# Optimization experiments

Measured on AMD Instinct MI355X. Metric: run time of the kernel, lower is better.

Reference implementation:

```python
import jax, jax.numpy as jnp
import numpy as np

EMBED_DIM = 1024
NUM_HEADS = 16
GQA = 4
KV_HEADS = NUM_HEADS // GQA          # 4
HEAD_DIM = EMBED_DIM // NUM_HEADS    # 64
KV_EMBED = KV_HEADS * HEAD_DIM       # 512
EPS = 1e-3
B, T = 2, 1024


def monotonic_attention(probs):
    """Many-to-many monotonic attention over sigmoid probs.

    probs: (..., Tq, Tk) in (0,1).
    Recurrence: phi[0] = onehot(key 0);
      phi[i, j] = p[i-1, j] * phi[i-1, j] + (1 - p[i, j-1]) * phi[i, j-1].
    The inner (j) recurrence is a first-order linear recurrence solved with
    an associative scan; the outer (i) recurrence uses lax.scan.
    """
    p = jnp.clip(probs, EPS, 1.0 - EPS)
    p_t = jnp.moveaxis(p, -2, 0)  # (Tq, ..., Tk)
    init = jnp.zeros(p_t.shape[1:], p.dtype).at[..., 0].set(1.0)

    def combine(x, y):
        A1, b1 = x
        A2, b2 = y
        return (A1 * A2, b1 * A2 + b2)

    def step(phi_prev, rows):
        p_prev, p_cur = rows
        a = phi_prev * p_prev                    # mass arriving from row above
        q = 1.0 - p_cur                          # stay-in-row (move right) prob
        A = jnp.concatenate([jnp.zeros_like(q[..., :1]), q[..., :-1]], axis=-1)
        _, phi = jax.lax.associative_scan(combine, (A, a), axis=-1)
        return phi, phi

    _, phis = jax.lax.scan(step, init, (p_t[:-1], p_t[1:]))
    phis = jnp.concatenate([init[None], phis], axis=0)  # (Tq, ..., Tk)
    return jnp.moveaxis(phis, 0, -2)


def setup_inputs() -> dict:
    key = jax.random.key(0)
    ks = jax.random.split(key, 5)
    scale_in = (2.0 / (EMBED_DIM + 2 * KV_EMBED + EMBED_DIM)) ** 0.5  # xavier-ish
    scale_out = (2.0 / (2 * EMBED_DIM)) ** 0.5
    return {
        "query": jax.random.normal(ks[0], (B, T, EMBED_DIM), jnp.float32),
        "key": jax.random.normal(ks[1], (B, T, EMBED_DIM), jnp.float32),
        "value": jax.random.normal(ks[2], (B, T, EMBED_DIM), jnp.float32),
        "in_proj_weight": jax.random.normal(ks[3], (EMBED_DIM + 2 * KV_EMBED, EMBED_DIM), jnp.float32) * scale_in,
        "in_proj_bias": jnp.zeros((EMBED_DIM + 2 * KV_EMBED,), jnp.float32),
        "out_proj_weight": jax.random.normal(ks[4], (EMBED_DIM, EMBED_DIM), jnp.float32) * scale_out,
        "out_proj_bias": jnp.zeros((EMBED_DIM,), jnp.float32),
    }


def reference(query, key, value, in_proj_weight, in_proj_bias, out_proj_weight, out_proj_bias):
    qw = in_proj_weight[:EMBED_DIM]
    kw = in_proj_weight[EMBED_DIM:EMBED_DIM + KV_EMBED]
    vw = in_proj_weight[EMBED_DIM + KV_EMBED:]
    qb = in_proj_bias[:EMBED_DIM]
    kb = in_proj_bias[EMBED_DIM:EMBED_DIM + KV_EMBED]
    vb = in_proj_bias[EMBED_DIM + KV_EMBED:]

    b, tq, _ = query.shape
    tk = key.shape[1]
    xq = query @ qw.T + qb   # (B, Tq, E)
    xk = key @ kw.T + kb     # (B, Tk, KV_EMBED)
    xv = value @ vw.T + vb   # (B, Tk, KV_EMBED)

    # (B, G, H, Tq, C) and (B, H, Tk, C)
    xq = xq.reshape(b, tq, GQA, KV_HEADS, HEAD_DIM).transpose(0, 2, 3, 1, 4)
    xk = xk.reshape(b, tk, KV_HEADS, HEAD_DIM).transpose(0, 2, 1, 3)
    xv = xv.reshape(b, tk, KV_HEADS, HEAD_DIM).transpose(0, 2, 1, 3)

    attn = jnp.einsum("bghqc,bhkc->bghqk", xq, xk)
    attn = monotonic_attention(jax.nn.sigmoid(attn))
    xo = jnp.einsum("bghqk,bhkc->bghqc", attn, xv)
    xo = xo.transpose(0, 3, 1, 2, 4).reshape(b, tq, EMBED_DIM)
    return xo @ out_proj_weight.T + out_proj_bias
```

## Files before the change

### kernel.cpp

```cpp
#include <hip/hip_runtime.h>
#include <cstddef>
#include <cstdint>

#define TSEQ 1024

typedef __attribute__((ext_vector_type(8))) short short8;
typedef __attribute__((ext_vector_type(4))) float floatx4;

static constexpr size_t OFF_XQ  = 0;
static constexpr size_t OFF_XK  = (size_t)2 * 1024 * 1024;
static constexpr size_t OFF_XVT = OFF_XK + (size_t)512 * 1024;
static constexpr size_t OFF_XO  = OFF_XVT + (size_t)512 * 1024;
static constexpr size_t OFF_P   = OFF_XO + (size_t)2 * 1024 * 1024;


__device__ __forceinline__ void cvt_hi_lo(float x, unsigned short& hi,
                                          unsigned short& lo) {
  unsigned u = __float_as_uint(x);
  unsigned rh = (u + 0x7FFFu + ((u >> 16) & 1u)) & 0xFFFF0000u;
  hi = (unsigned short)(rh >> 16);
  float xl = x - __uint_as_float(rh);
  unsigned ul = __float_as_uint(xl);
  unsigned rl = ul + 0x7FFFu + ((ul >> 16) & 1u);
  lo = (unsigned short)(rl >> 16);
}

__device__ __forceinline__ int diagrow(int r, int cblk) {
  return ((((r >> 2) + cblk) & 255) << 2) | (r & 3);
}

typedef unsigned short lds_tile_t[40];

template <int EPI, int ADIAG, int CDIAG>
__device__ __forceinline__ void mfma_nt_core(
    const float* __restrict__ A, int lda,
    const float* __restrict__ B, int ldb,
    float* __restrict__ C, int ldc, int K,
    const float* __restrict__ bias,
    int bm, int bn,
    lds_tile_t* __restrict__ Ah, lds_tile_t* __restrict__ Al,
    lds_tile_t* __restrict__ Bh, lds_tile_t* __restrict__ Bl)
{
  const int tid  = threadIdx.x;
  const int lane = tid & 63;
  const int wave = tid >> 6;
  const int m16  = lane & 15;
  const int quad = lane >> 4;

  const int srow = tid >> 2;
  const int skq  = (tid & 3) << 3;

  floatx4 acc[4];
#pragma unroll
  for (int c = 0; c < 4; ++c) acc[c] = (floatx4){0.f, 0.f, 0.f, 0.f};

  for (int k0 = 0; k0 < K; k0 += 32) {
    {
      const int kq = k0 + skq;
      int arow = bm + srow;
      if (ADIAG) arow = diagrow(arow, kq >> 4);
      const float* ap = A + (size_t)arow * lda + kq;
      const float* bp = B + (size_t)(bn + srow) * ldb + kq;
      float av[8] __attribute__((aligned(16)));
      float bv[8] __attribute__((aligned(16)));
      *(float4*)&av[0] = *(const float4*)(ap);
      *(float4*)&av[4] = *(const float4*)(ap + 4);
      *(float4*)&bv[0] = *(const float4*)(bp);
      *(float4*)&bv[4] = *(const float4*)(bp + 4);
      short8 vah, valo, vbh, vblo;
#pragma unroll
      for (int e = 0; e < 8; ++e) {
        unsigned short h, l;
        cvt_hi_lo(av[e], h, l);
        vah[e] = (short)h; valo[e] = (short)l;
        cvt_hi_lo(bv[e], h, l);
        vbh[e] = (short)h; vblo[e] = (short)l;
      }
      *(short8*)&Ah[srow][skq] = vah;
      *(short8*)&Al[srow][skq] = valo;
      *(short8*)&Bh[srow][skq] = vbh;
      *(short8*)&Bl[srow][skq] = vblo;
    }
    __syncthreads();

    const int arow = (wave << 4) + m16;
    const short8 a_h = *(const short8*)&Ah[arow][quad << 3];
    const short8 a_l = *(const short8*)&Al[arow][quad << 3];
#pragma unroll
    for (int c = 0; c < 4; ++c) {
      const int brow = (c << 4) + m16;
      const short8 b_h = *(const short8*)&Bh[brow][quad << 3];
      const short8 b_l = *(const short8*)&Bl[brow][quad << 3];
      acc[c] = __builtin_amdgcn_mfma_f32_16x16x32_bf16(a_h, b_h, acc[c], 0, 0, 0);
      acc[c] = __builtin_amdgcn_mfma_f32_16x16x32_bf16(a_h, b_l, acc[c], 0, 0, 0);
      acc[c] = __builtin_amdgcn_mfma_f32_16x16x32_bf16(a_l, b_h, acc[c], 0, 0, 0);
    }
    __syncthreads();
  }

#pragma unroll
  for (int c = 0; c < 4; ++c) {
#pragma unroll
    for (int r = 0; r < 4; ++r) {
      const int row = (wave << 4) + (quad << 2) + r;
      const int col = (c << 4) + m16;
      float v = acc[c][r];
      if (EPI == 0) { if (bias) v += bias[bn + col]; }
      if (EPI == 1) { v += bias[bm + row]; }
      if (EPI == 2) {
        v = 1.0f / (1.0f + __expf(v));
        v = fminf(fmaxf(v, 0.001f), 0.999f);
      }
      int crow = bm + row;
      if (CDIAG) crow = diagrow(crow, (bn + col) >> 4);
      C[(size_t)crow * ldc + (bn + col)] = v;
    }
  }
}

#define DECL_GEMM_SMEM                                          \
  __shared__ __align__(16) unsigned short Ah[64][40];           \
  __shared__ __align__(16) unsigned short Al[64][40];           \
  __shared__ __align__(16) unsigned short Bh[64][40];           \
  __shared__ __align__(16) unsigned short Bl[64][40];

__global__ __launch_bounds__(256) void inproj_k(
    const float* __restrict__ query, const float* __restrict__ key,
    const float* __restrict__ value, const float* __restrict__ ipw,
    const float* __restrict__ ipb,
    float* __restrict__ XQ, float* __restrict__ XK, float* __restrict__ XVt)
{
  DECL_GEMM_SMEM
  const int id = blockIdx.x;
  if (id < 512) {
    mfma_nt_core<0, 0, 0>(query, 1024, ipw, 1024, XQ, 1024, 1024, ipb,
                          (id >> 4) << 6, (id & 15) << 6, Ah, Al, Bh, Bl);
  } else if (id < 640) {
    const int j = id - 512;
    mfma_nt_core<0, 0, 0>(key, 1024, ipw + ((size_t)1 << 20), 1024,
                          XK, 256, 1024, ipb + 1024,
                          (j >> 2) << 6, (j & 3) << 6, Ah, Al, Bh, Bl);
  } else {
    const int j = id - 640;
    const int b = j >> 6;
    mfma_nt_core<1, 0, 0>(ipw + (size_t)1280 * 1024, 1024,
                          value + ((size_t)b << 20), 1024,
                          XVt + (size_t)b * 256 * 1024, 1024, 1024,
                          ipb + 1280,
                          ((j >> 4) & 3) << 6, (j & 15) << 6, Ah, Al, Bh, Bl);
  }
}

__global__ __launch_bounds__(256) void gemm_nt_mfma_k(
    const float* __restrict__ A, int lda, const float* __restrict__ W, int ldw,
    const float* __restrict__ bias, float* __restrict__ C, int ldc, int K)
{
  DECL_GEMM_SMEM
  mfma_nt_core<0, 0, 0>(A, lda, W, ldw, C, ldc, K, bias,
                        blockIdx.y << 6, blockIdx.x << 6, Ah, Al, Bh, Bl);
}

__global__ __launch_bounds__(256) void scores_mfma_k(
    const float* __restrict__ XQ, const float* __restrict__ XK,
    float* __restrict__ P)
{
  DECL_GEMM_SMEM
  const int z = blockIdx.z;
  const int b = z >> 4;
  mfma_nt_core<2, 0, 1>(XQ + ((size_t)b << 20) + ((size_t)(z & 15) << 6), 1024,
                        XK + (size_t)b * TSEQ * 256 + ((size_t)(z & 3) << 6), 256,
                        P + ((size_t)z << 20), 1024, 64, nullptr,
                        blockIdx.y << 6, blockIdx.x << 6, Ah, Al, Bh, Bl);
}

__global__ __launch_bounds__(256) void pv_mfma_k(
    const float* __restrict__ P, const float* __restrict__ XVt,
    float* __restrict__ XO)
{
  DECL_GEMM_SMEM
  const int z = blockIdx.z;
  const int b = z >> 4;
  mfma_nt_core<0, 1, 0>(P + ((size_t)z << 20), 1024,
                        XVt + (size_t)b * 256 * 1024 + (size_t)(z & 3) * 64 * 1024, 1024,
                        XO + ((size_t)b << 20) + ((size_t)(z & 15) << 6), 1024,
                        1024, nullptr,
                        blockIdx.y << 6, blockIdx.x << 6, Ah, Al, Bh, Bl);
}

__global__ __launch_bounds__(64) void mono_rec_k(float* __restrict__ P)
{
  const int z = blockIdx.x;
  float* __restrict__ Pz = P + ((size_t)z << 20);
  const int t = threadIdx.x;
  const int col0 = t << 4;

  float b[16];
#pragma unroll
  for (int c = 0; c < 16; ++c) b[c] = 0.0f;
  float phi15h[4], q15h[4];
#pragma unroll
  for (int k = 0; k < 4; ++k) { phi15h[k] = 0.0f; q15h[k] = 0.0f; }

  float pA[4][16], pB[4][16];

#pragma unroll
  for (int k = 0; k < 4; ++k) {
    const float* lp = Pz + (k << 10) + col0;
#pragma unroll
    for (int q = 0; q < 4; ++q)
      *(float4*)&pA[k][4 * q] = *(const float4*)(lp + 4 * q);
  }

  auto step = [&](int s, float (&pcur)[4][16], float (&pnext)[4][16]) {
    float phiL[4], qL[4];
#pragma unroll
    for (int k = 0; k < 4; ++k) {
      phiL[k] = __shfl_up(phi15h[k], 1);
      qL[k]   = __shfl_up(q15h[k], 1);
    }

    {
      const float* np = Pz + ((size_t)((s + 1) & 255) << 12) + col0;
#pragma unroll
      for (int k = 0; k < 4; ++k)
#pragma unroll
        for (int q = 0; q < 4; ++q)
          *(float4*)&pnext[k][4 * q] = *(const float4*)(np + (k << 10) + 4 * q);
    }

    const int g = s - t;
    if (g >= 0 && g < 256) {
      float* sp = Pz + ((size_t)(s & 255) << 12) + col0;
      float phi[16];
#pragma unroll
      for (int k = 0; k < 4; ++k) {
        const float* qk = pcur[k];
        if (g == 0 && k == 0) {
#pragma unroll
          for (int c = 0; c < 16; ++c) phi[c] = 0.0f;
          if (t == 0) phi[0] = 1.0f;
        } else {
          const float H0 = (t == 0) ? 0.0f : qL[k];
          float x = fmaf(H0, phiL[k], b[0]);
          phi[0] = x;
#pragma unroll
          for (int c = 1; c < 16; ++c) {
            x = fmaf(qk[c - 1], x, b[c]);
            phi[c] = x;
          }
        }
#pragma unroll
        for (int c = 0; c < 16; ++c) b[c] = fmaf(-qk[c], phi[c], phi[c]);
        q15h[k]   = qk[15];
        phi15h[k] = phi[15];
#pragma unroll
        for (int q = 0; q < 4; ++q)
          *(float4*)(sp + (k << 10) + 4 * q) = *(float4*)&phi[4 * q];
      }
    }
  };

  for (int s0 = 0; s0 < 320; s0 += 2) {
    step(s0, pA, pB);
    step(s0 + 1, pB, pA);
  }
}

extern "C" void kernel_launch(void* const* d_in, const int* in_sizes, int n_in,
                              void* d_out, int out_size, void* d_ws, size_t ws_size,
                              hipStream_t stream)
{
  const float* query = (const float*)d_in[0];
  const float* key   = (const float*)d_in[1];
  const float* value = (const float*)d_in[2];
  const float* ipw   = (const float*)d_in[3];
  const float* ipb   = (const float*)d_in[4];
  const float* opw   = (const float*)d_in[5];
  const float* opb   = (const float*)d_in[6];
  float* out = (float*)d_out;
  float* ws  = (float*)d_ws;

  float* XQ  = ws + OFF_XQ;
  float* XK  = ws + OFF_XK;
  float* XVt = ws + OFF_XVT;
  float* XO  = ws + OFF_XO;
  float* P   = ws + OFF_P;

  inproj_k<<<dim3(768), 256, 0, stream>>>(
      query, key, value, ipw, ipb, XQ, XK, XVt);

  scores_mfma_k<<<dim3(16, 16, 32), 256, 0, stream>>>(XQ, XK, P);

  mono_rec_k<<<dim3(32), dim3(64), 0, stream>>>(P);

  pv_mfma_k<<<dim3(1, 16, 32), 256, 0, stream>>>(P, XVt, XO);

  gemm_nt_mfma_k<<<dim3(16, 32), 256, 0, stream>>>(
      XO, 1024, opw, 1024, opb, out, 1024, 1024);
}
```

Measured before the change: 483.9 us.

## Widen monotonic recurrence to 256 threads with LDS wave-boundary handoff

The monotonic-attention wavefront kernel now runs 256 threads per head, with each thread owning 4 columns instead of 16. Carries between waves pass through double-buffered shared memory guarded by a block barrier on every step. The diagonal storage layout of P changes from 16-column to 4-column granularity, and the scores and PV GEMM loaders are adjusted to match. The goal is more parallelism and a shorter serial chain per step, at the cost of more wavefront steps (512 instead of 320) and a barrier in each one.

Result: slower. 495.2 us (+2.3%).

```diff
diff --git a/kernel.cpp b/kernel.cpp
--- a/kernel.cpp
+++ b/kernel.cpp
@@ -25,8 +25,8 @@
   lo = (unsigned short)(rl >> 16);
 }
 
-__device__ __forceinline__ int diagrow(int r, int cblk) {
-  return ((((r >> 2) + cblk) & 255) << 2) | (r & 3);
+__device__ __forceinline__ int diagrow4(int r, int c) {
+  return ((((r >> 2) + (c >> 2)) & 255) << 2) | (r & 3);
 }
 
 typedef unsigned short lds_tile_t[40];
@@ -57,14 +57,23 @@
   for (int k0 = 0; k0 < K; k0 += 32) {
     {
       const int kq = k0 + skq;
-      int arow = bm + srow;
-      if (ADIAG) arow = diagrow(arow, kq >> 4);
-      const float* ap = A + (size_t)arow * lda + kq;
+      const float* ap;
+      const float* ap2;
+      if (ADIAG) {
+        const int r  = bm + srow;
+        const int a0 = diagrow4(r, kq);
+        const int a1 = diagrow4(r, kq + 4);
+        ap  = A + (size_t)a0 * lda + kq;
+        ap2 = A + (size_t)a1 * lda + (kq + 4);
+      } else {
+        ap  = A + (size_t)(bm + srow) * lda + kq;
+        ap2 = ap + 4;
+      }
       const float* bp = B + (size_t)(bn + srow) * ldb + kq;
       float av[8] __attribute__((aligned(16)));
       float bv[8] __attribute__((aligned(16)));
       *(float4*)&av[0] = *(const float4*)(ap);
-      *(float4*)&av[4] = *(const float4*)(ap + 4);
+      *(float4*)&av[4] = *(const float4*)(ap2);
       *(float4*)&bv[0] = *(const float4*)(bp);
       *(float4*)&bv[4] = *(const float4*)(bp + 4);
       short8 vah, valo, vbh, vblo;
@@ -112,7 +121,7 @@
         v = fminf(fmaxf(v, 0.001f), 0.999f);
       }
       int crow = bm + row;
-      if (CDIAG) crow = diagrow(crow, (bn + col) >> 4);
+      if (CDIAG) crow = diagrow4(bm + row, bn + col);
       C[(size_t)crow * ldc + (bn + col)] = v;
     }
   }
@@ -187,80 +196,103 @@
                         blockIdx.y << 6, blockIdx.x << 6, Ah, Al, Bh, Bl);
 }
 
-__global__ __launch_bounds__(64) void mono_rec_k(float* __restrict__ P)
+#define MONO_BAR() do {                                          \
+    asm volatile("s_waitcnt lgkmcnt(0)" ::: "memory");           \
+    __builtin_amdgcn_sched_barrier(0);                           \
+    asm volatile("s_barrier" ::: "memory");                      \
+    __builtin_amdgcn_sched_barrier(0);                           \
+  } while (0)
+
+__global__ __launch_bounds__(256, 1) void mono_rec_k(float* __restrict__ P)
 {
   const int z = blockIdx.x;
   float* __restrict__ Pz = P + ((size_t)z << 20);
-  const int t = threadIdx.x;
-  const int col0 = t << 4;
-
-  float b[16];
-#pragma unroll
-  for (int c = 0; c < 16; ++c) b[c] = 0.0f;
-  float phi15h[4], q15h[4];
-#pragma unroll
-  for (int k = 0; k < 4; ++k) { phi15h[k] = 0.0f; q15h[k] = 0.0f; }
-
-  float pA[4][16], pB[4][16];
-
-#pragma unroll
-  for (int k = 0; k < 4; ++k) {
-    const float* lp = Pz + (k << 10) + col0;
-#pragma unroll
-    for (int q = 0; q < 4; ++q)
-      *(float4*)&pA[k][4 * q] = *(const float4*)(lp + 4 * q);
-  }
-
-  auto step = [&](int s, float (&pcur)[4][16], float (&pnext)[4][16]) {
+  const int tid = threadIdx.x;
+  const int u = tid;
+  const int w = tid >> 6;
+  const int l = tid & 63;
+
+  __shared__ float BndP[2][3][4];
+  __shared__ float BndQ[2][3][4];
+
+  float b[4];
+#pragma unroll
+  for (int c = 0; c < 4; ++c) b[c] = 0.0f;
+  float phi3h[4], q3h[4];
+#pragma unroll
+  for (int k = 0; k < 4; ++k) { phi3h[k] = 0.0f; q3h[k] = 0.0f; }
+
+  float pA[4][4], pB[4][4];
+
+#pragma unroll
+  for (int k = 0; k < 4; ++k)
+    *(float4*)&pA[k][0] = *(const float4*)(Pz + (k << 10) + (u << 2));
+
+  auto step = [&](int s, float (&pcur)[4][4], float (&pnext)[4][4]) {
     float phiL[4], qL[4];
 #pragma unroll
     for (int k = 0; k < 4; ++k) {
-      phiL[k] = __shfl_up(phi15h[k], 1);
-      qL[k]   = __shfl_up(q15h[k], 1);
+      phiL[k] = __shfl_up(phi3h[k], 1);
+      qL[k]   = __shfl_up(q3h[k], 1);
+    }
+    if (l == 0 && w > 0) {
+#pragma unroll
+      for (int k = 0; k < 4; ++k) {
+        phiL[k] = BndP[(s + 1) & 1][w - 1][k];
+        qL[k]   = BndQ[(s + 1) & 1][w - 1][k];
+      }
     }
 
     {
-      const float* np = Pz + ((size_t)((s + 1) & 255) << 12) + col0;
+      const float* np = Pz + ((size_t)((s + 1) & 255) << 12) + (u << 2);
 #pragma unroll
       for (int k = 0; k < 4; ++k)
-#pragma unroll
-        for (int q = 0; q < 4; ++q)
-          *(float4*)&pnext[k][4 * q] = *(const float4*)(np + (k << 10) + 4 * q);
-    }
-
-    const int g = s - t;
+        *(float4*)&pnext[k][0] = *(const float4*)(np + (k << 10));
+    }
+
+    const int g = s - u;
     if (g >= 0 && g < 256) {
-      float* sp = Pz + ((size_t)(s & 255) << 12) + col0;
-      float phi[16];
+      float phim[4][4];
 #pragma unroll
       for (int k = 0; k < 4; ++k) {
         const float* qk = pcur[k];
+        float* phi = phim[k];
         if (g == 0 && k == 0) {
 #pragma unroll
-          for (int c = 0; c < 16; ++c) phi[c] = 0.0f;
-          if (t == 0) phi[0] = 1.0f;
+          for (int c = 0; c < 4; ++c) phi[c] = 0.0f;
+          if (u == 0) phi[0] = 1.0f;
         } else {
-          const float H0 = (t == 0) ? 0.0f : qL[k];
+          const float H0 = (u == 0) ? 0.0f : qL[k];
           float x = fmaf(H0, phiL[k], b[0]);
           phi[0] = x;
 #pragma unroll
-          for (int c = 1; c < 16; ++c) {
+          for (int c = 1; c < 4; ++c) {
             x = fmaf(qk[c - 1], x, b[c]);
             phi[c] = x;
           }
         }
 #pragma unroll
-        for (int c = 0; c < 16; ++c) b[c] = fmaf(-qk[c], phi[c], phi[c]);
-        q15h[k]   = qk[15];
-        phi15h[k] = phi[15];
-#pragma unroll
-        for (int q = 0; q < 4; ++q)
-          *(float4*)(sp + (k << 10) + 4 * q) = *(float4*)&phi[4 * q];
-      }
-    }
+        for (int c = 0; c < 4; ++c) b[c] = fmaf(-qk[c], phi[c], phi[c]);
+        q3h[k]   = qk[3];
+        phi3h[k] = phi[3];
+      }
+      float* sp = Pz + ((size_t)(s & 255) << 12) + (u << 2);
+#pragma unroll
+      for (int k = 0; k < 4; ++k)
+        *(float4*)(sp + (k << 10)) = *(float4*)&phim[k][0];
+    }
+
+    if (l == 63 && w < 3) {
+#pragma unroll
+      for (int k = 0; k < 4; ++k) {
+        BndP[s & 1][w][k] = phi3h[k];
+        BndQ[s & 1][w][k] = q3h[k];
+      }
+    }
+    MONO_BAR();
   };
 
-  for (int s0 = 0; s0 < 320; s0 += 2) {
+  for (int s0 = 0; s0 < 512; s0 += 2) {
     step(s0, pA, pB);
     step(s0 + 1, pB, pA);
   }
@@ -291,7 +323,7 @@
 
   scores_mfma_k<<<dim3(16, 16, 32), 256, 0, stream>>>(XQ, XK, P);
 
-  mono_rec_k<<<dim3(32), dim3(64), 0, stream>>>(P);
+  mono_rec_k<<<dim3(32), dim3(256), 0, stream>>>(P);
 
   pv_mfma_k<<<dim3(1, 16, 32), 256, 0, stream>>>(P, XVt, XO);
 
```
